# Optimization experiments

Measured on AMD Instinct MI355X. Metric: run time of the kernel, lower is better.

The kernel has to match this reference:

```python
import jax, jax.numpy as jnp
import numpy as np

K, B, C, T, D, H = 4, 1024, 128, 64, 64, 4  # timeframes, batch, in-feat, seq(=embed!), embed, heads
HD = D // H
EPS = 1e-5


def setup_inputs() -> dict:
    key = jax.random.key(0)
    ks = jax.random.split(key, 8)
    s = lambda k, shape: jax.random.normal(k, shape, dtype=jnp.float32) * 0.05
    return {
        "feats": jax.random.normal(ks[0], (K, B, C, T), dtype=jnp.float32),
        "proj_w": s(ks[1], (K, D, C)),
        "proj_b": jnp.zeros((K, D), jnp.float32),
        "wq": s(ks[2], (K, D, D)),
        "wk": s(ks[3], (K, D, D)),
        "wv": s(ks[4], (K, D, D)),
        "bq": jnp.zeros((K, D), jnp.float32),
        "bk": jnp.zeros((K, D), jnp.float32),
        "bv": jnp.zeros((K, D), jnp.float32),
        "wo": s(ks[5], (K, D, D)),
        "bo": jnp.zeros((K, D), jnp.float32),
        "ng": jnp.ones((K, D), jnp.float32),
        "nb": jnp.zeros((K, D), jnp.float32),
        "tfw": jnp.full((K,), 1.0 / K, jnp.float32),
        "fg": jnp.ones((K * D,), jnp.float32),
        "fb": jnp.zeros((K * D,), jnp.float32),
    }


def _ln(x, g, b):
    m = x.mean(-1, keepdims=True)
    v = ((x - m) ** 2).mean(-1, keepdims=True)
    return (x - m) * jax.lax.rsqrt(v + EPS) * g + b


def reference(feats, proj_w, proj_b, wq, wk, wv, bq, bk, bv, wo, bo, ng, nb, tfw, fg, fb):
    # per-timeframe Linear on channel axis: [K,B,C,T] -> [K,B,D,T]
    proj = jnp.einsum('kbct,kdc->kbdt', feats, proj_w) + proj_b[:, None, :, None]
    ctx4 = jnp.transpose(proj, (1, 0, 2, 3))              # [B,K,D,T] (torch.stack dim=1)
    ctx = ctx4.reshape(B * D, K, T)                       # replicates torch .view(B*T,K,D); needs T==D
    N = B * D
    scale = 1.0 / np.sqrt(HD)
    outs = []
    for i in range(K):  # small fixed loop over K=4 distinct attention blocks
        q_in = ctx[:, i]                                  # [N,D] query = i-th row
        q = (q_in @ wq[i].T + bq[i]).reshape(N, H, HD)
        k = (ctx @ wk[i].T + bk[i]).reshape(N, K, H, HD)
        v = (ctx @ wv[i].T + bv[i]).reshape(N, K, H, HD)
        sc = jnp.einsum('nhe,nkhe->nhk', q, k) * scale    # [N,H,K]
        a = jax.nn.softmax(sc, axis=-1)
        o = jnp.einsum('nhk,nkhe->nhe', a, v).reshape(N, D)
        o = o @ wo[i].T + bo[i]
        outs.append(_ln(o + q_in, ng[i], nb[i]))          # residual + per-tf LayerNorm
    w = jax.nn.softmax(tfw)
    comb = jnp.stack(outs, axis=1) * w[None, :, None]     # [N,K,D] weighted fusion
    fused = comb.reshape(B, D, K * D)                     # torch .view(B,T,K*D)
    return _ln(fused, fg, fb)
```

## Files before the change

### kernel.cpp

```cpp
#include <hip/hip_runtime.h>
#include <math.h>

#define EPSV 1e-5f

typedef __attribute__((ext_vector_type(8))) short short8;
typedef __attribute__((ext_vector_type(4))) float float4v;
typedef __attribute__((ext_vector_type(4))) unsigned short ushort4v;

__device__ __forceinline__ unsigned short f2bf(float f) {
  unsigned int x = __float_as_uint(f);
  return (unsigned short)((x + 0x7fffu + ((x >> 16) & 1u)) >> 16);
}
__device__ __forceinline__ float bf2f(unsigned short u) {
  return __uint_as_float(((unsigned int)u) << 16);
}
__device__ __forceinline__ float wave_sum64(float v) {
  v += __shfl_xor(v, 1);
  v += __shfl_xor(v, 2);
  v += __shfl_xor(v, 4);
  v += __shfl_xor(v, 8);
  v += __shfl_xor(v, 16);
  v += __shfl_xor(v, 32);
  return v;
}
__device__ __forceinline__ float group16_sum(float v) {
  v += __shfl_xor(v, 1);
  v += __shfl_xor(v, 2);
  v += __shfl_xor(v, 4);
  v += __shfl_xor(v, 8);
  return v;
}
__device__ __forceinline__ void lds_fence() {
  asm volatile("s_waitcnt lgkmcnt(0)" ::: "memory");
}

__global__ __launch_bounds__(256) void prep_kernel(
    const float* __restrict__ pw, const float* __restrict__ wq,
    const float* __restrict__ wk, const float* __restrict__ wv,
    const float* __restrict__ wo, unsigned short* __restrict__ wph,
    unsigned short* __restrict__ wpl, unsigned short* __restrict__ wb) {
  int idx = blockIdx.x * 256 + threadIdx.x;
  if (idx < 32768) {
    float f = pw[idx];
    unsigned short h = f2bf(f);
    wph[idx] = h;
    wpl[idx] = f2bf(f - bf2f(h));
  } else {
    int e = idx - 32768;
    int mat = e >> 14, i = (e >> 12) & 3, r = e & 4095;
    const float* src = (mat == 0) ? wq : (mat == 1) ? wk : (mat == 2) ? wv : wo;
    wb[((i * 4 + mat) << 12) + r] = f2bf(src[(i << 12) + r]);
  }
}

__global__ __launch_bounds__(256, 2) void fused_kernel(
    const float* __restrict__ feats, const unsigned short* __restrict__ wph,
    const unsigned short* __restrict__ wpl, const float* __restrict__ pb,
    const unsigned short* __restrict__ wb,
    const float* __restrict__ bq, const float* __restrict__ bk,
    const float* __restrict__ bv, const float* __restrict__ bo,
    const float* __restrict__ ng, const float* __restrict__ nb,
    const float* __restrict__ tfw, const float* __restrict__ fg,
    const float* __restrict__ fb, float* __restrict__ out) {
  __shared__ __align__(16) unsigned short POOL[2 * 64 * 136];
  __shared__ __align__(16) unsigned short CTP[64 * 264];
  __shared__ __align__(16) unsigned short OSP[4][16 * 72];

  unsigned short* const FH = POOL;
  unsigned short* const FL = POOL + 64 * 136;
  unsigned short* const CMB = POOL;

  int tid = threadIdx.x;
  int w = tid >> 6, l = tid & 63;
  int l15 = l & 15, lq = l >> 4;
  const float4v zf = {0.0f, 0.0f, 0.0f, 0.0f};

#pragma unroll 1
  for (int k = 0; k < 4; ++k) {
    __syncthreads();
    const float* fsrc = feats + ((size_t)k * 1024 + blockIdx.x) * 8192;
#pragma unroll
    for (int it = 0; it < 4; ++it) {
      int e = it * 256 + tid;
      int t = e & 63;
      int cg = e >> 6;
      float fv[8];
#pragma unroll
      for (int q = 0; q < 8; ++q) fv[q] = fsrc[(cg * 8 + q) * 64 + t];
      short8 hv, lv;
#pragma unroll
      for (int q = 0; q < 8; ++q) {
        unsigned short h = f2bf(fv[q]);
        hv[q] = (short)h;
        lv[q] = (short)f2bf(fv[q] - bf2f(h));
      }
      *(short8*)&FH[t * 136 + cg * 8] = hv;
      *(short8*)&FL[t * 136 + cg * 8] = lv;
    }
    __syncthreads();

    float4v acc[4] = {zf, zf, zf, zf};
    const unsigned short* whp = wph + k * 8192 + (w * 16 + l15) * 128 + lq * 8;
    const unsigned short* wlp = wpl + k * 8192 + (w * 16 + l15) * 128 + lq * 8;

    __builtin_amdgcn_s_setprio(1);
#pragma unroll
    for (int kc = 0; kc < 4; ++kc) {
      short8 ah = *(const short8*)&whp[kc * 32];
      short8 al = *(const short8*)&wlp[kc * 32];
#pragma unroll
      for (int nt = 0; nt < 4; ++nt) {
        short8 bh = *(const short8*)&FH[(nt * 16 + l15) * 136 + kc * 32 + lq * 8];
        short8 bl = *(const short8*)&FL[(nt * 16 + l15) * 136 + kc * 32 + lq * 8];
        acc[nt] = __builtin_amdgcn_mfma_f32_16x16x32_bf16(ah, bh, acc[nt], 0, 0, 0);
        acc[nt] = __builtin_amdgcn_mfma_f32_16x16x32_bf16(ah, bl, acc[nt], 0, 0, 0);
        acc[nt] = __builtin_amdgcn_mfma_f32_16x16x32_bf16(al, bh, acc[nt], 0, 0, 0);
      }
    }
    __builtin_amdgcn_s_setprio(0);

    float pbv[4];
#pragma unroll
    for (int r = 0; r < 4; ++r) pbv[r] = pb[k * 64 + w * 16 + lq * 4 + r];

#pragma unroll
    for (int nt = 0; nt < 4; ++nt)
#pragma unroll
      for (int r = 0; r < 4; ++r)
        CTP[(k * 16 + w * 4 + lq) * 264 + r * 64 + nt * 16 + l15] =
            f2bf(acc[nt][r] + pbv[r]);
  }
  __syncthreads();

  float tf0 = tfw[0], tf1 = tfw[1], tf2 = tfw[2], tf3 = tfw[3];
  float tm = fmaxf(fmaxf(tf0, tf1), fmaxf(tf2, tf3));
  float te0 = __expf(tf0 - tm), te1 = __expf(tf1 - tm);
  float te2 = __expf(tf2 - tm), te3 = __expf(tf3 - tm);
  float tden = te0 + te1 + te2 + te3;

  const unsigned short* arow = &CTP[(w * 16 + l15) * 264];

#pragma unroll 1
  for (int i = 0; i < 4; ++i) {
#define WFRAG(m, nt, s)                                                        \
  (*(const short8*)&wb[((i * 4 + (m)) << 12) + ((nt)*16 + l15) * 64 +          \
                       (s)*32 + lq * 8])

    float wi = ((i == 0) ? te0 : (i == 1) ? te1 : (i == 2) ? te2 : te3) / tden;

    float bqv[4], bkv[4], bvv[4];
#pragma unroll
    for (int nt = 0; nt < 4; ++nt) {
      int d = i * 64 + nt * 16 + l15;
      bqv[nt] = bq[d]; bkv[nt] = bk[d]; bvv[nt] = bv[d];
    }

    float4v qacc[4] = {zf, zf, zf, zf};
    __builtin_amdgcn_s_setprio(1);
#pragma unroll
    for (int s = 0; s < 2; ++s) {
      short8 af = *(const short8*)&arow[i * 64 + s * 32 + lq * 8];
#pragma unroll
      for (int nt = 0; nt < 4; ++nt)
        qacc[nt] = __builtin_amdgcn_mfma_f32_16x16x32_bf16(af, WFRAG(0, nt, s),
                                                           qacc[nt], 0, 0, 0);
    }
    __builtin_amdgcn_s_setprio(0);
#pragma unroll
    for (int nt = 0; nt < 4; ++nt)
#pragma unroll
      for (int r = 0; r < 4; ++r) qacc[nt][r] += bqv[nt];

    short8 kf[2][4], vf[2][4];
#pragma unroll
    for (int s = 0; s < 2; ++s)
#pragma unroll
      for (int nt = 0; nt < 4; ++nt) {
        kf[s][nt] = WFRAG(1, nt, s);
        vf[s][nt] = WFRAG(2, nt, s);
      }

    float4v oacc[4] = {zf, zf, zf, zf};
    float lsum[4][4] = {{0,0,0,0},{0,0,0,0},{0,0,0,0},{0,0,0,0}};

#pragma unroll 1
    for (int j = 0; j < 4; ++j) {
      float4v kacc[4] = {zf, zf, zf, zf};
      float4v vacc[4] = {zf, zf, zf, zf};
      __builtin_amdgcn_s_setprio(1);
#pragma unroll
      for (int s = 0; s < 2; ++s) {
        short8 af = *(const short8*)&arow[j * 64 + s * 32 + lq * 8];
#pragma unroll
        for (int nt = 0; nt < 4; ++nt) {
          kacc[nt] = __builtin_amdgcn_mfma_f32_16x16x32_bf16(af, kf[s][nt],
                                                             kacc[nt], 0, 0, 0);
          vacc[nt] = __builtin_amdgcn_mfma_f32_16x16x32_bf16(af, vf[s][nt],
                                                             vacc[nt], 0, 0, 0);
        }
      }
      __builtin_amdgcn_s_setprio(0);
#pragma unroll
      for (int nt = 0; nt < 4; ++nt)
#pragma unroll
        for (int r = 0; r < 4; ++r) {
          float p = qacc[nt][r] * (kacc[nt][r] + bkv[nt]);
          p = group16_sum(p) * 0.25f;
          float e = __expf(p);
          lsum[nt][r] += e;
          oacc[nt][r] += e * (vacc[nt][r] + bvv[nt]);
        }
    }

    lds_fence();
#pragma unroll
    for (int nt = 0; nt < 4; ++nt)
#pragma unroll
      for (int r = 0; r < 4; ++r)
        OSP[w][(lq * 4 + r) * 72 + nt * 16 + l15] = f2bf(oacc[nt][r] / lsum[nt][r]);
    lds_fence();

    float4v o2[4] = {zf, zf, zf, zf};
    __builtin_amdgcn_s_setprio(1);
#pragma unroll
    for (int s = 0; s < 2; ++s) {
      short8 af = *(const short8*)&OSP[w][l15 * 72 + s * 32 + lq * 8];
#pragma unroll
      for (int nt = 0; nt < 4; ++nt)
        o2[nt] = __builtin_amdgcn_mfma_f32_16x16x32_bf16(af, WFRAG(3, nt, s),
                                                         o2[nt], 0, 0, 0);
    }
    __builtin_amdgcn_s_setprio(0);

    float bov[4], ngv[4], nbv[4];
#pragma unroll
    for (int nt = 0; nt < 4; ++nt) {
      int d = i * 64 + nt * 16 + l15;
      bov[nt] = bo[d]; ngv[nt] = ng[d]; nbv[nt] = nb[d];
    }

    float rr[4][4];
#pragma unroll
    for (int nt = 0; nt < 4; ++nt)
#pragma unroll
      for (int r = 0; r < 4; ++r) {
        float qin = bf2f(CTP[(w * 16 + lq * 4 + r) * 264 + i * 64 + nt * 16 + l15]);
        rr[nt][r] = o2[nt][r] + bov[nt] + qin;
      }

#pragma unroll
    for (int r = 0; r < 4; ++r) {
      float sm = group16_sum(rr[0][r] + rr[1][r] + rr[2][r] + rr[3][r]) * (1.0f / 64.0f);
      float vs = 0.0f;
#pragma unroll
      for (int nt = 0; nt < 4; ++nt) { float dx = rr[nt][r] - sm; vs += dx * dx; }
      vs = group16_sum(vs) * (1.0f / 64.0f);
      float inv = rsqrtf(vs + EPSV);
      int rowl = w * 16 + lq * 4 + r;
#pragma unroll
      for (int nt = 0; nt < 4; ++nt) {
        float val = wi * ((rr[nt][r] - sm) * inv * ngv[nt] + nbv[nt]);
        CMB[rowl * 256 + i * 64 + nt * 16 + l15] = f2bf(val);
      }
    }
#undef WFRAG
  }

  lds_fence();
  float4 g = *(const float4*)&fg[l * 4];
  float4 bb = *(const float4*)&fb[l * 4];
#pragma unroll 1
  for (int rr = 0; rr < 16; ++rr) {
    int rowl = w * 16 + rr;
    ushort4v pk = *(const ushort4v*)&CMB[rowl * 256 + l * 4];
    float vx = bf2f(pk.x), vy = bf2f(pk.y), vz = bf2f(pk.z), vw = bf2f(pk.w);
    float mean = wave_sum64(vx + vy + vz + vw) * (1.0f / 256.0f);
    float dx = vx - mean, dy = vy - mean, dz = vz - mean, dw = vw - mean;
    float var = wave_sum64(dx * dx + dy * dy + dz * dz + dw * dw) * (1.0f / 256.0f);
    float inv = rsqrtf(var + EPSV);
    float4 o;
    o.x = dx * inv * g.x + bb.x;
    o.y = dy * inv * g.y + bb.y;
    o.z = dz * inv * g.z + bb.z;
    o.w = dw * inv * g.w + bb.w;
    *(float4*)&out[((size_t)blockIdx.x * 64 + rowl) * 256 + l * 4] = o;
  }
}

extern "C" void kernel_launch(void* const* d_in, const int* in_sizes, int n_in,
                              void* d_out, int out_size, void* d_ws, size_t ws_size,
                              hipStream_t stream) {
  const float* feats  = (const float*)d_in[0];
  const float* proj_w = (const float*)d_in[1];
  const float* proj_b = (const float*)d_in[2];
  const float* wq  = (const float*)d_in[3];
  const float* wk  = (const float*)d_in[4];
  const float* wv  = (const float*)d_in[5];
  const float* bq  = (const float*)d_in[6];
  const float* bk  = (const float*)d_in[7];
  const float* bv  = (const float*)d_in[8];
  const float* wo  = (const float*)d_in[9];
  const float* bo  = (const float*)d_in[10];
  const float* ng  = (const float*)d_in[11];
  const float* nb  = (const float*)d_in[12];
  const float* tfw = (const float*)d_in[13];
  const float* fg  = (const float*)d_in[14];
  const float* fb  = (const float*)d_in[15];
  float* out = (float*)d_out;

  unsigned short* wph = (unsigned short*)d_ws;
  unsigned short* wpl = wph + 32768;
  unsigned short* wb  = wpl + 32768;

  prep_kernel<<<384, 256, 0, stream>>>(proj_w, wq, wk, wv, wo, wph, wpl, wb);
  fused_kernel<<<1024, 256, 0, stream>>>(feats, wph, wpl, proj_b, wb,
                                         bq, bk, bv, bo, ng, nb, tfw,
                                         fg, fb, out);
}
```

Baseline: 343.5 us.

## Assign one timeframe per wave in projection stage to remove block barriers

The projection GEMM is restructured so each wave owns one timeframe k and computes the full 64x64 output tile. It stages its features in a private, XOR-swizzled LDS slice, 32 channels at a time. This replaces the block-wide __syncthreads with wave-local LDS fences, and the combine buffer becomes per-wave too. In exchange, accumulator registers grow 4x and each wave loads more projection weight fragments from global memory, which may hurt occupancy.

```diff
diff --git a/kernel.cpp b/kernel.cpp
--- a/kernel.cpp
+++ b/kernel.cpp
@@ -62,75 +62,86 @@
     const float* __restrict__ ng, const float* __restrict__ nb,
     const float* __restrict__ tfw, const float* __restrict__ fg,
     const float* __restrict__ fb, float* __restrict__ out) {
-  __shared__ __align__(16) unsigned short POOL[2 * 64 * 136];
+  __shared__ __align__(16) unsigned short POOL[4 * 4096];
   __shared__ __align__(16) unsigned short CTP[64 * 264];
   __shared__ __align__(16) unsigned short OSP[4][16 * 72];
-
-  unsigned short* const FH = POOL;
-  unsigned short* const FL = POOL + 64 * 136;
-  unsigned short* const CMB = POOL;
 
   int tid = threadIdx.x;
   int w = tid >> 6, l = tid & 63;
   int l15 = l & 15, lq = l >> 4;
   const float4v zf = {0.0f, 0.0f, 0.0f, 0.0f};
 
+  unsigned short* const WPOOL = POOL + w * 4096;
+  unsigned short* const FHW = WPOOL;
+  unsigned short* const FLW = WPOOL + 2048;
+  unsigned short* const CMBW = WPOOL;
+
+  {
+    const float* fsrc = feats + ((size_t)w * 1024 + blockIdx.x) * 8192;
+    const unsigned short* whp = wph + w * 8192;
+    const unsigned short* wlp = wpl + w * 8192;
+
+    float4v acc[4][4];
+#pragma unroll
+    for (int mt = 0; mt < 4; ++mt)
+#pragma unroll
+      for (int nt = 0; nt < 4; ++nt) acc[mt][nt] = zf;
+
+    int sur = lq ^ ((l15 >> 1) & 3);
+
 #pragma unroll 1
-  for (int k = 0; k < 4; ++k) {
-    __syncthreads();
-    const float* fsrc = feats + ((size_t)k * 1024 + blockIdx.x) * 8192;
-#pragma unroll
-    for (int it = 0; it < 4; ++it) {
-      int e = it * 256 + tid;
-      int t = e & 63;
-      int cg = e >> 6;
-      float fv[8];
-#pragma unroll
-      for (int q = 0; q < 8; ++q) fv[q] = fsrc[(cg * 8 + q) * 64 + t];
-      short8 hv, lv;
-#pragma unroll
-      for (int q = 0; q < 8; ++q) {
-        unsigned short h = f2bf(fv[q]);
-        hv[q] = (short)h;
-        lv[q] = (short)f2bf(fv[q] - bf2f(h));
-      }
-      *(short8*)&FH[t * 136 + cg * 8] = hv;
-      *(short8*)&FL[t * 136 + cg * 8] = lv;
-    }
-    __syncthreads();
-
-    float4v acc[4] = {zf, zf, zf, zf};
-    const unsigned short* whp = wph + k * 8192 + (w * 16 + l15) * 128 + lq * 8;
-    const unsigned short* wlp = wpl + k * 8192 + (w * 16 + l15) * 128 + lq * 8;
-
-    __builtin_amdgcn_s_setprio(1);
-#pragma unroll
     for (int kc = 0; kc < 4; ++kc) {
-      short8 ah = *(const short8*)&whp[kc * 32];
-      short8 al = *(const short8*)&wlp[kc * 32];
+      lds_fence();
+#pragma unroll
+      for (int u = 0; u < 4; ++u) {
+        float fv[8];
+#pragma unroll
+        for (int q = 0; q < 8; ++q)
+          fv[q] = fsrc[(kc * 32 + u * 8 + q) * 64 + l];
+        short8 hv, lv;
+#pragma unroll
+        for (int q = 0; q < 8; ++q) {
+          unsigned short h = f2bf(fv[q]);
+          hv[q] = (short)h;
+          lv[q] = (short)f2bf(fv[q] - bf2f(h));
+        }
+        int su = u ^ ((l >> 1) & 3);
+        *(short8*)&FHW[l * 32 + su * 8] = hv;
+        *(short8*)&FLW[l * 32 + su * 8] = lv;
+      }
+      lds_fence();
+
+      __builtin_amdgcn_s_setprio(1);
+#pragma unroll
+      for (int mt = 0; mt < 4; ++mt) {
+        short8 ah = *(const short8*)&whp[(mt * 16 + l15) * 128 + kc * 32 + lq * 8];
+        short8 al = *(const short8*)&wlp[(mt * 16 + l15) * 128 + kc * 32 + lq * 8];
+#pragma unroll
+        for (int nt = 0; nt < 4; ++nt) {
+          short8 bh = *(const short8*)&FHW[(nt * 16 + l15) * 32 + sur * 8];
+          short8 bl = *(const short8*)&FLW[(nt * 16 + l15) * 32 + sur * 8];
+          acc[mt][nt] = __builtin_amdgcn_mfma_f32_16x16x32_bf16(ah, bh, acc[mt][nt], 0, 0, 0);
+          acc[mt][nt] = __builtin_amdgcn_mfma_f32_16x16x32_bf16(ah, bl, acc[mt][nt], 0, 0, 0);
+          acc[mt][nt] = __builtin_amdgcn_mfma_f32_16x16x32_bf16(al, bh, acc[mt][nt], 0, 0, 0);
+        }
+      }
+      __builtin_amdgcn_s_setprio(0);
+    }
+
+#pragma unroll
+    for (int mt = 0; mt < 4; ++mt) {
+      float4 pbm = *(const float4*)&pb[w * 64 + mt * 16 + lq * 4];
 #pragma unroll
       for (int nt = 0; nt < 4; ++nt) {
-        short8 bh = *(const short8*)&FH[(nt * 16 + l15) * 136 + kc * 32 + lq * 8];
-        short8 bl = *(const short8*)&FL[(nt * 16 + l15) * 136 + kc * 32 + lq * 8];
-        acc[nt] = __builtin_amdgcn_mfma_f32_16x16x32_bf16(ah, bh, acc[nt], 0, 0, 0);
-        acc[nt] = __builtin_amdgcn_mfma_f32_16x16x32_bf16(ah, bl, acc[nt], 0, 0, 0);
-        acc[nt] = __builtin_amdgcn_mfma_f32_16x16x32_bf16(al, bh, acc[nt], 0, 0, 0);
-      }
-    }
-    __builtin_amdgcn_s_setprio(0);
-
-    float pbv[4];
-#pragma unroll
-    for (int r = 0; r < 4; ++r) pbv[r] = pb[k * 64 + w * 16 + lq * 4 + r];
-
-#pragma unroll
-    for (int nt = 0; nt < 4; ++nt)
-#pragma unroll
-      for (int r = 0; r < 4; ++r)
-        CTP[(k * 16 + w * 4 + lq) * 264 + r * 64 + nt * 16 + l15] =
-            f2bf(acc[nt][r] + pbv[r]);
+        float pr[4] = {pbm.x, pbm.y, pbm.z, pbm.w};
+#pragma unroll
+        for (int r = 0; r < 4; ++r)
+          CTP[(w * 16 + mt * 4 + lq) * 264 + r * 64 + nt * 16 + l15] =
+              f2bf(acc[mt][nt][r] + pr[r]);
+      }
+    }
   }
-  __syncthreads();
+  lds_fence();
 
   float tf0 = tfw[0], tf1 = tfw[1], tf2 = tfw[2], tf3 = tfw[3];
   float tm = fmaxf(fmaxf(tf0, tf1), fmaxf(tf2, tf3));
@@ -256,11 +267,11 @@
       for (int nt = 0; nt < 4; ++nt) { float dx = rr[nt][r] - sm; vs += dx * dx; }
       vs = group16_sum(vs) * (1.0f / 64.0f);
       float inv = rsqrtf(vs + EPSV);
-      int rowl = w * 16 + lq * 4 + r;
+      int lr = lq * 4 + r;
 #pragma unroll
       for (int nt = 0; nt < 4; ++nt) {
         float val = wi * ((rr[nt][r] - sm) * inv * ngv[nt] + nbv[nt]);
-        CMB[rowl * 256 + i * 64 + nt * 16 + l15] = f2bf(val);
+        CMBW[lr * 256 + i * 64 + nt * 16 + l15] = f2bf(val);
       }
     }
 #undef WFRAG
@@ -271,8 +282,7 @@
   float4 bb = *(const float4*)&fb[l * 4];
 #pragma unroll 1
   for (int rr = 0; rr < 16; ++rr) {
-    int rowl = w * 16 + rr;
-    ushort4v pk = *(const ushort4v*)&CMB[rowl * 256 + l * 4];
+    ushort4v pk = *(const ushort4v*)&CMBW[rr * 256 + l * 4];
     float vx = bf2f(pk.x), vy = bf2f(pk.y), vz = bf2f(pk.z), vw = bf2f(pk.w);
     float mean = wave_sum64(vx + vy + vz + vw) * (1.0f / 256.0f);
     float dx = vx - mean, dy = vy - mean, dz = vz - mean, dw = vw - mean;
@@ -283,7 +293,7 @@
     o.y = dy * inv * g.y + bb.y;
     o.z = dz * inv * g.z + bb.z;
     o.w = dw * inv * g.w + bb.w;
-    *(float4*)&out[((size_t)blockIdx.x * 64 + rowl) * 256 + l * 4] = o;
+    *(float4*)&out[((size_t)blockIdx.x * 64 + w * 16 + rr) * 256 + l * 4] = o;
   }
 }
 
```

After: 339.6 us. No clear change (-1.2%).
